# Kernel tuning notes

Measured on AMD Instinct MI355X. Metric: run time of the kernel, lower is better.

Reference implementation:

```python
import jax, jax.numpy as jnp
import numpy as np

D = 256; H = 8; FF = 1024; Q = 128; C = 512; B = 4
HD = D // H

def _ln(x, g, b):
    m = x.mean(-1, keepdims=True)
    v = ((x - m) ** 2).mean(-1, keepdims=True)
    return (x - m) / jnp.sqrt(v + 1e-5) * g + b

def _mha(q, k, v, in_w, in_b, out_w, out_b):
    # q,k,v: (L,B,D) / (S,B,D); in_w: (3D,D) packed q|k|v as in torch MHA
    qp = q @ in_w[:D].T + in_b[:D]
    kp = k @ in_w[D:2*D].T + in_b[D:2*D]
    vp = v @ in_w[2*D:].T + in_b[2*D:]
    L, Bb, _ = qp.shape; S = kp.shape[0]
    qh = qp.reshape(L, Bb, H, HD)
    kh = kp.reshape(S, Bb, H, HD)
    vh = vp.reshape(S, Bb, H, HD)
    scores = jnp.einsum('lbhd,sbhd->bhls', qh, kh) / np.sqrt(HD).astype(np.float32)
    a = jax.nn.softmax(scores, axis=-1)
    o = jnp.einsum('bhls,sbhd->lbhd', a, vh).reshape(L, Bb, D)
    return o @ out_w.T + out_b

def setup_inputs() -> dict:
    key = jax.random.key(0)
    ks = jax.random.split(key, 30)
    def p(k, shape, s=0.02):
        return jax.random.normal(k, shape, jnp.float32) * s
    return {
        'tgt': jax.random.normal(ks[0], (Q, B, D), jnp.float32),
        'memory': jax.random.normal(ks[1], (C, B, D), jnp.float32),
        'query_pos': jax.random.normal(ks[2], (Q, B, D), jnp.float32),
        'relative_pos': jax.random.normal(ks[3], (Q, C, B, D), jnp.float32),
        'ln1_g': jnp.ones((D,), jnp.float32), 'ln1_b': jnp.zeros((D,), jnp.float32),
        'ln2_g': jnp.ones((D,), jnp.float32), 'ln2_b': jnp.zeros((D,), jnp.float32),
        'ln3_g': jnp.ones((D,), jnp.float32), 'ln3_b': jnp.zeros((D,), jnp.float32),
        'in_proj_w': p(ks[4], (3 * D, D)), 'in_proj_b': jnp.zeros((3 * D,), jnp.float32),
        'attn_out_w': p(ks[5], (D, D)), 'attn_out_b': jnp.zeros((D,), jnp.float32),
        'mlp1_w': p(ks[6], (D, D)), 'mlp1_b': jnp.zeros((D,), jnp.float32),
        'mlp2_w': p(ks[7], (D, D)), 'mlp2_b': jnp.zeros((D,), jnp.float32),
        'v_w': p(ks[8], (D, D)), 'v_b': jnp.zeros((D,), jnp.float32),
        'o_w': p(ks[9], (D, D)), 'o_b': jnp.zeros((D,), jnp.float32),
        'ff1_w': p(ks[10], (FF, D)), 'ff1_b': jnp.zeros((FF,), jnp.float32),
        'ff2_w': p(ks[11], (D, FF)), 'ff2_b': jnp.zeros((D,), jnp.float32),
    }

def reference(tgt, memory, query_pos, relative_pos,
              ln1_g, ln1_b, ln2_g, ln2_b, ln3_g, ln3_b,
              in_proj_w, in_proj_b, attn_out_w, attn_out_b,
              mlp1_w, mlp1_b, mlp2_w, mlp2_b,
              v_w, v_b, o_w, o_b, ff1_w, ff1_b, ff2_w, ff2_b):
    # pre-norm self-attention (dropout = identity in eval)
    tgt2 = _ln(tgt, ln1_g, ln1_b)
    qk = tgt2 + query_pos
    sa = _mha(qk, qk, tgt2, in_proj_w, in_proj_b, attn_out_w, attn_out_b)
    tgt = tgt + sa
    # relation-attention branch
    tgt2 = _ln(tgt, ln2_g, ln2_b)                       # (Q,B,D)
    x = tgt2[:, None, :, :] - memory[None, :, :, :] + relative_pos  # (Q,C,B,D)
    h = jax.nn.relu(x @ mlp1_w.T + mlp1_b)
    sim = h @ mlp2_w.T + mlp2_b                          # (Q,C,B,D)
    attn = jax.nn.softmax(sim / np.sqrt(D).astype(np.float32), axis=1)
    v2 = (memory[None, :, :, :] + relative_pos) @ v_w.T + v_b
    t = jnp.einsum('qcbf,qcbf->qbf', attn, v2)           # (Q,B,D)
    t = jax.nn.relu(t @ o_w.T + o_b)
    tgt = t + tgt2
    # FFN
    tgt2 = _ln(tgt, ln3_g, ln3_b)
    ff = jax.nn.relu(tgt2 @ ff1_w.T + ff1_b) @ ff2_w.T + ff2_b
    return tgt + ff
```

## Files before the change

### kernel.cpp

```cpp
#include <hip/hip_runtime.h>
#include <hip/hip_bf16.h>
#include <cstdint>
#include <cstddef>

#define DEV __device__ __forceinline__

typedef __attribute__((ext_vector_type(8))) short short8;
typedef __attribute__((ext_vector_type(4))) float f32x4;

constexpr int Dm  = 256;
constexpr int Qn  = 128;
constexpr int Cn  = 512;
constexpr int Bn  = 4;

DEV unsigned short f2bf(float f){
  unsigned int u = __builtin_bit_cast(unsigned int, f);
  u += 0x7fffu + ((u >> 16) & 1u);
  return (unsigned short)(u >> 16);
}
DEV float bfl(unsigned int u){ return __builtin_bit_cast(float, u << 16); }
DEV float bfh(unsigned int u){ return __builtin_bit_cast(float, u & 0xffff0000u); }
DEV unsigned int pk2(float a, float b){
  return (unsigned int)f2bf(a) | ((unsigned int)f2bf(b) << 16);
}
DEV unsigned int corr2(unsigned int x, unsigned int m, unsigned int t){
  return pk2(bfl(x) + bfl(m) - bfl(t), bfh(x) + bfh(m) - bfh(t));
}

DEV f32x4 mfma16(short8 a, short8 b, f32x4 c){
  return __builtin_amdgcn_mfma_f32_16x16x32_bf16(a, b, c, 0, 0, 0);
}

DEV short8 ldfrag(const unsigned short* buf, int rowbytes, int row0, int ks, int l){
  int r = row0 + (l & 15);
  int byte = (ks * 64 + ((l >> 4) * 16)) ^ ((r & 7) << 4);
  return *(const short8*)((const char*)buf + r * rowbytes + byte);
}

DEV void gload_lds16(const void* g, void* lds){
  __builtin_amdgcn_global_load_lds(
      (const __attribute__((address_space(1))) unsigned int*)g,
      (__attribute__((address_space(3))) unsigned int*)lds, 16, 0, 0);
}

DEV void packw(unsigned short* dst, const float* src, int j){
  int f = j >> 8, d = j & 255;
  int d8 = d >> 3, e = d & 7;
  int byte = (d8 * 16) ^ ((f & 15) << 4);
  dst[f * 256 + (byte >> 1) + e] = f2bf(src[j]);
}

__global__ __launch_bounds__(256) void conv_all_kernel(
    const float* inw, unsigned short* inw_bf,
    const float* aow, unsigned short* aow_bf,
    const float* ow,  unsigned short* ow_bf,
    const float* f1w, unsigned short* f1w_bf,
    const float* f2w, unsigned short* f2w_bf,
    const float* m1w, unsigned short* w1pk,
    const float* m2w, unsigned short* w2pk,
    const float* vw,  unsigned short* wvpk,
    const float* memp, unsigned short* m2r)
{
  const int total = 196608 + 65536 + 65536 + 262144 + 262144 + 3 * 65536 + 524288;
  for (int i = blockIdx.x * 256 + threadIdx.x; i < total; i += gridDim.x * 256){
    int j = i;
    if (j < 196608){ inw_bf[j] = f2bf(inw[j]); continue; } j -= 196608;
    if (j < 65536) { aow_bf[j] = f2bf(aow[j]); continue; } j -= 65536;
    if (j < 65536) { ow_bf[j]  = f2bf(ow[j]);  continue; } j -= 65536;
    if (j < 262144){ f1w_bf[j] = f2bf(f1w[j]); continue; } j -= 262144;
    if (j < 262144){ f2w_bf[j] = f2bf(f2w[j]); continue; } j -= 262144;
    if (j < 65536) { packw(w1pk, m1w, j); continue; } j -= 65536;
    if (j < 65536) { packw(w2pk, m2w, j); continue; } j -= 65536;
    if (j < 65536) { packw(wvpk, vw, j);  continue; } j -= 65536;
    int d = j & 255, c = (j >> 8) & 511, b2 = j >> 17;
    m2r[j] = f2bf(2.f * memp[((size_t)c * 4 + b2) * 256 + d]);
  }
}

__global__ __launch_bounds__(256) void xprep_kernel(
    const float* __restrict__ rel, const float* __restrict__ memp,
    const float* __restrict__ t22, unsigned short* __restrict__ xg)
{
  const int total = Qn * Cn * Bn * 32;
  for (int i = blockIdx.x * 256 + threadIdx.x; i < total; i += gridDim.x * 256){
    int d8 = i & 31;
    int b  = (i >> 5) & 3;
    int c  = (i >> 7) & 511;
    int q  = i >> 16;
    const float4* rp = (const float4*)(rel + (size_t)i * 8);
    float4 r0 = rp[0], r1 = rp[1];
    const float4* mp = (const float4*)(memp + ((size_t)(c * 4 + b) * 256 + d8 * 8));
    float4 m0 = mp[0], m1 = mp[1];
    const float4* tp = (const float4*)(t22 + ((size_t)(q * 4 + b) * 256 + d8 * 8));
    float4 t0 = tp[0], t1 = tp[1];
    uint4 o;
    o.x = pk2(t0.x - m0.x + r0.x, t0.y - m0.y + r0.y);
    o.y = pk2(t0.z - m0.z + r0.z, t0.w - m0.w + r0.w);
    o.z = pk2(t1.x - m1.x + r1.x, t1.y - m1.y + r1.y);
    o.w = pk2(t1.z - m1.z + r1.z, t1.w - m1.w + r1.w);
    size_t byte = ((size_t)(q * 4 + b) * 512 + c) * 512 + ((d8 * 16) ^ ((c & 15) << 4));
    *(uint4*)((char*)xg + byte) = o;
  }
}

__global__ __launch_bounds__(256) void ln_kernel(
    const float* __restrict__ in, const float* __restrict__ g, const float* __restrict__ bt,
    const float* __restrict__ addp,
    float* __restrict__ outF, unsigned short* __restrict__ outA, unsigned short* __restrict__ outB)
{
  const int r = blockIdx.x, t = threadIdx.x;
  float x = in[(size_t)r * 256 + t];
  float s = x, s2 = x * x;
  #pragma unroll
  for (int m = 1; m < 64; m <<= 1){ s += __shfl_xor(s, m, 64); s2 += __shfl_xor(s2, m, 64); }
  __shared__ float ls[8];
  int w = t >> 6, l = t & 63;
  if (l == 0){ ls[w] = s; ls[4 + w] = s2; }
  __syncthreads();
  s  = ls[0] + ls[1] + ls[2] + ls[3];
  s2 = ls[4] + ls[5] + ls[6] + ls[7];
  float mean = s * (1.f / 256.f);
  float var  = s2 * (1.f / 256.f) - mean * mean;
  float y = (x - mean) * rsqrtf(var + 1e-5f) * g[t] + bt[t];
  size_t o = (size_t)r * 256 + t;
  if (outF) outF[o] = y;
  if (outA) outA[o] = f2bf(y);
  if (outB) outB[o] = f2bf(y + addp[o]);
}

__global__ __launch_bounds__(256, 4) void gemm_kernel(
    const unsigned short* __restrict__ A, const unsigned short* __restrict__ W,
    const float* __restrict__ bias, const float* __restrict__ resid,
    float* __restrict__ Cf, unsigned short* __restrict__ Cb,
    int M, int N, int K, float alpha, int relu)
{
  __shared__ unsigned short As[64 * 64];
  __shared__ unsigned short Ws[64 * 64];
  const int tid = threadIdx.x;
  const int l = tid & 63;
  const int w = tid >> 6;
  const int wm = w >> 1, wn = w & 1;
  const int bm = blockIdx.x * 64, bn = blockIdx.y * 64;
  f32x4 acc[2][2] = {{{0,0,0,0},{0,0,0,0}},{{0,0,0,0},{0,0,0,0}}};

  for (int kc = 0; kc < K; kc += 64){
    __syncthreads();
    #pragma unroll
    for (int i = 0; i < 2; ++i){
      int idx = tid + i * 256;
      int r = idx >> 3, s = idx & 7;
      int byte = (s * 16) ^ ((r & 7) << 4);
      *(short8*)((char*)As + r * 128 + byte) = *(const short8*)(A + (size_t)(bm + r) * K + kc + s * 8);
      *(short8*)((char*)Ws + r * 128 + byte) = *(const short8*)(W + (size_t)(bn + r) * K + kc + s * 8);
    }
    __syncthreads();
    #pragma unroll
    for (int ks = 0; ks < 2; ++ks){
      short8 af[2], bf[2];
      af[0] = ldfrag(As, 128, wm * 32,      ks, l);
      af[1] = ldfrag(As, 128, wm * 32 + 16, ks, l);
      bf[0] = ldfrag(Ws, 128, wn * 32,      ks, l);
      bf[1] = ldfrag(Ws, 128, wn * 32 + 16, ks, l);
      #pragma unroll
      for (int i = 0; i < 2; ++i)
        #pragma unroll
        for (int j = 0; j < 2; ++j)
          acc[i][j] = mfma16(af[i], bf[j], acc[i][j]);
    }
  }
  #pragma unroll
  for (int i = 0; i < 2; ++i)
  #pragma unroll
  for (int j = 0; j < 2; ++j){
    int col = bn + wn * 32 + j * 16 + (l & 15);
    float bv = bias ? bias[col] : 0.f;
    #pragma unroll
    for (int u = 0; u < 4; ++u){
      int row = bm + wm * 32 + i * 16 + ((l >> 4) << 2) + u;
      float v = alpha * acc[i][j][u] + bv;
      if (relu) v = fmaxf(v, 0.f);
      if (resid) v += resid[(size_t)row * N + col];
      if (Cf) Cf[(size_t)row * N + col] = v;
      if (Cb) Cb[(size_t)row * N + col] = f2bf(v);
    }
  }
}

__global__ __launch_bounds__(256) void attn_kernel(
    const float* __restrict__ qkp, const float* __restrict__ vp,
    unsigned short* __restrict__ attn_o)
{
  __shared__ float ks[128][33];
  __shared__ float vs[128][33];
  __shared__ float sc[128][129];
  const int bh = blockIdx.x;
  const int b = bh >> 3, h = bh & 7;
  const int tid = threadIdx.x;
  const int lrow = tid >> 1;
  const int half = tid & 1;
  {
    int s = tid >> 1;
    int d0 = half * 16;
    const float* kp = qkp + ((size_t)s * Bn + b) * 512 + 256 + h * 32 + d0;
    const float* vv = vp  + ((size_t)s * Bn + b) * 256 +       h * 32 + d0;
    #pragma unroll
    for (int d = 0; d < 16; d += 4){
      *(float4*)&ks[s][d0 + d] = *(const float4*)(kp + d);
      *(float4*)&vs[s][d0 + d] = *(const float4*)(vv + d);
    }
  }
  __syncthreads();
  float qv[32];
  const float* qp = qkp + ((size_t)lrow * Bn + b) * 512 + h * 32;
  #pragma unroll
  for (int d = 0; d < 32; ++d) qv[d] = qp[d];
  const float scale = 0.17677669529663687f;
  float mloc = -1e30f;
  for (int s2 = 0; s2 < 64; ++s2){
    int s = half * 64 + s2;
    float dot = 0.f;
    #pragma unroll
    for (int d = 0; d < 32; ++d) dot += qv[d] * ks[s][d];
    dot *= scale;
    sc[lrow][s] = dot;
    mloc = fmaxf(mloc, dot);
  }
  float m = fmaxf(mloc, __shfl_xor(mloc, 1, 64));
  float sum = 0.f;
  for (int s2 = 0; s2 < 64; ++s2){
    int s = half * 64 + s2;
    float e = __expf(sc[lrow][s] - m);
    sum += e;
    sc[lrow][s] = e;
  }
  sum += __shfl_xor(sum, 1, 64);
  float inv = 1.f / sum;
  float o[32];
  #pragma unroll
  for (int d = 0; d < 32; ++d) o[d] = 0.f;
  for (int s2 = 0; s2 < 64; ++s2){
    int s = half * 64 + s2;
    float e = sc[lrow][s];
    #pragma unroll
    for (int d = 0; d < 32; ++d) o[d] += e * vs[s][d];
  }
  #pragma unroll
  for (int d = 0; d < 32; ++d){
    o[d] += __shfl_xor(o[d], 1, 64);
    o[d] *= inv;
  }
  unsigned short* op = attn_o + ((size_t)lrow * Bn + b) * 256 + h * 32 + half * 16;
  #pragma unroll
  for (int d = 0; d < 16; ++d) op[d] = f2bf(o[half * 16 + d]);
}

template<int MODE>
__global__ __launch_bounds__(1024, 4) void relpass_kernel(
    const unsigned short* src, const unsigned short* __restrict__ Wg,
    const float* __restrict__ bias, unsigned short* dst,
    const unsigned short* __restrict__ m2r, const unsigned short* __restrict__ t22b,
    const unsigned short* simsrc)
{
  __shared__ unsigned short Wt[65536];
  __shared__ unsigned short xb[8192];
  const int qb = blockIdx.x;
  const int b = qb & 3;
  const int tid = threadIdx.x;
  const int w = tid >> 6, l = tid & 63;
  const int ch2 = w >> 3, fb = w & 7;
  const int l15 = l & 15, lg = l >> 4;

  #pragma unroll
  for (int i = 0; i < 8; ++i){
    int base = w * 64 + i * 1024;
    gload_lds16((const char*)Wg + ((size_t)base + l) * 16, (char*)Wt + (size_t)base * 16);
  }

  const int row = tid >> 5, d8 = tid & 31;
  const int toff = row * 512 + ((d8 * 16) ^ ((row & 15) << 4));
  const char* srcp = (const char*)src + (size_t)qb * 262144;

  uint4 stg = *(const uint4*)(srcp + toff);
  uint4 m2c, t2c;
  if constexpr (MODE == 2){
    m2c = *(const uint4*)((const char*)m2r + ((size_t)(b * 512 + row) * 512) + d8 * 16);
    t2c = *(const uint4*)((const char*)t22b + (size_t)qb * 512 + d8 * 16);
  }
  asm volatile("s_waitcnt vmcnt(0)" ::: "memory");
  if constexpr (MODE == 2){
    stg.x = corr2(stg.x, m2c.x, t2c.x);
    stg.y = corr2(stg.y, m2c.y, t2c.y);
    stg.z = corr2(stg.z, m2c.z, t2c.z);
    stg.w = corr2(stg.w, m2c.w, t2c.w);
  }
  *(uint4*)((char*)xb + toff) = stg;
  __syncthreads();

  float bv[2][4];
  #pragma unroll
  for (int j = 0; j < 2; ++j)
    #pragma unroll
    for (int u = 0; u < 4; ++u)
      bv[j][u] = bias[fb * 32 + j * 16 + lg * 4 + u];

  float ta[2][4], la[2][4];
  if constexpr (MODE == 2){
    #pragma unroll
    for (int j = 0; j < 2; ++j)
      #pragma unroll
      for (int u = 0; u < 4; ++u){ ta[j][u] = 0.f; la[j][u] = 0.f; }
  }

  const int r = ch2 * 16 + l15;
  for (int t = 0; t < 16; ++t){
    if (t < 15){
      stg = *(const uint4*)(srcp + (size_t)(t + 1) * 16384 + toff);
      if constexpr (MODE == 2)
        m2c = *(const uint4*)((const char*)m2r + ((size_t)(b * 512 + (t + 1) * 32 + row) * 512) + d8 * 16);
    }
    uint4 simv;
    if constexpr (MODE == 2)
      simv = *(const uint4*)((const char*)simsrc + (size_t)qb * 262144 + (size_t)t * 16384 + (size_t)(w * 64 + l) * 16);

    f32x4 acc[2] = {{0,0,0,0},{0,0,0,0}};
    #pragma unroll
    for (int kc = 0; kc < 8; ++kc){
      short8 bx = *(const short8*)((const char*)xb + r * 512 + ((kc * 64 + lg * 16) ^ ((r & 15) << 4)));
      #pragma unroll
      for (int j = 0; j < 2; ++j){
        int f = fb * 32 + j * 16 + l15;
        short8 aw = *(const short8*)((const char*)Wt + f * 512 + ((kc * 64 + lg * 16) ^ ((f & 15) << 4)));
        acc[j] = mfma16(aw, bx, acc[j]);
      }
    }

    if constexpr (MODE == 0){
      int c = t * 32 + r;
      size_t rowb = (size_t)qb * 262144 + (size_t)c * 512;
      #pragma unroll
      for (int j = 0; j < 2; ++j){
        uint2 pk;
        pk.x = pk2(fmaxf(acc[j][0] + bv[j][0], 0.f), fmaxf(acc[j][1] + bv[j][1], 0.f));
        pk.y = pk2(fmaxf(acc[j][2] + bv[j][2], 0.f), fmaxf(acc[j][3] + bv[j][3], 0.f));
        int inrow = (fb * 64 + j * 32 + lg * 8) ^ ((c & 15) << 4);
        *(uint2*)((char*)dst + rowb + inrow) = pk;
      }
    } else if constexpr (MODE == 1){
      uint4 d;
      d.x = pk2((acc[0][0] + bv[0][0]) * 0.0625f, (acc[0][1] + bv[0][1]) * 0.0625f);
      d.y = pk2((acc[0][2] + bv[0][2]) * 0.0625f, (acc[0][3] + bv[0][3]) * 0.0625f);
      d.z = pk2((acc[1][0] + bv[1][0]) * 0.0625f, (acc[1][1] + bv[1][1]) * 0.0625f);
      d.w = pk2((acc[1][2] + bv[1][2]) * 0.0625f, (acc[1][3] + bv[1][3]) * 0.0625f);
      *(uint4*)((char*)dst + (size_t)qb * 262144 + (size_t)t * 16384 + (size_t)(w * 64 + l) * 16) = d;
    } else {
      const unsigned int sv[4] = {simv.x, simv.y, simv.z, simv.w};
      #pragma unroll
      for (int j = 0; j < 2; ++j)
        #pragma unroll
        for (int p = 0; p < 2; ++p){
          unsigned int s2 = sv[j * 2 + p];
          float e0 = __expf(bfl(s2)), e1 = __expf(bfh(s2));
          float v0 = acc[j][p * 2 + 0] + bv[j][p * 2 + 0];
          float v1 = acc[j][p * 2 + 1] + bv[j][p * 2 + 1];
          ta[j][p * 2 + 0] += e0 * v0;  la[j][p * 2 + 0] += e0;
          ta[j][p * 2 + 1] += e1 * v1;  la[j][p * 2 + 1] += e1;
        }
    }

    if (t < 15){
      __syncthreads();
      if constexpr (MODE == 2){
        stg.x = corr2(stg.x, m2c.x, t2c.x);
        stg.y = corr2(stg.y, m2c.y, t2c.y);
        stg.z = corr2(stg.z, m2c.z, t2c.z);
        stg.w = corr2(stg.w, m2c.w, t2c.w);
      }
      *(uint4*)((char*)xb + toff) = stg;
      __syncthreads();
    }
  }

  if constexpr (MODE == 2){
    #pragma unroll
    for (int j = 0; j < 2; ++j)
      #pragma unroll
      for (int u = 0; u < 4; ++u){
        #pragma unroll
        for (int m = 1; m <= 8; m <<= 1){
          ta[j][u] += __shfl_xor(ta[j][u], m, 64);
          la[j][u] += __shfl_xor(la[j][u], m, 64);
        }
      }
    __syncthreads();
    float* bufT = (float*)xb;
    float* bufL = bufT + 512;
    if (l15 == 0){
      #pragma unroll
      for (int j = 0; j < 2; ++j)
        #pragma unroll
        for (int u = 0; u < 4; ++u){
          int f = fb * 32 + j * 16 + lg * 4 + u;
          bufT[ch2 * 256 + f] = ta[j][u];
          bufL[ch2 * 256 + f] = la[j][u];
        }
    }
    __syncthreads();
    if (tid < 256){
      float T = bufT[tid] + bufT[256 + tid];
      float L = bufL[tid] + bufL[256 + tid];
      dst[(size_t)qb * 256 + tid] = f2bf(T / L);
    }
  }
}

extern "C" void kernel_launch(void* const* d_in, const int* in_sizes, int n_in,
                              void* d_out, int out_size, void* d_ws, size_t ws_size,
                              hipStream_t stream)
{
  const float* tgt  = (const float*)d_in[0];
  const float* mem  = (const float*)d_in[1];
  const float* qpos = (const float*)d_in[2];
  const float* rel  = (const float*)d_in[3];
  const float* ln1g = (const float*)d_in[4];
  const float* ln1b = (const float*)d_in[5];
  const float* ln2g = (const float*)d_in[6];
  const float* ln2b = (const float*)d_in[7];
  const float* ln3g = (const float*)d_in[8];
  const float* ln3b = (const float*)d_in[9];
  const float* inw  = (const float*)d_in[10];
  const float* inb  = (const float*)d_in[11];
  const float* aow  = (const float*)d_in[12];
  const float* aob  = (const float*)d_in[13];
  const float* m1w  = (const float*)d_in[14];
  const float* m1b  = (const float*)d_in[15];
  const float* m2w  = (const float*)d_in[16];
  const float* m2b  = (const float*)d_in[17];
  const float* vw   = (const float*)d_in[18];
  const float* vb   = (const float*)d_in[19];
  const float* ow   = (const float*)d_in[20];
  const float* ob   = (const float*)d_in[21];
  const float* f1w  = (const float*)d_in[22];
  const float* f1b  = (const float*)d_in[23];
  const float* f2w  = (const float*)d_in[24];
  const float* f2b  = (const float*)d_in[25];

  char* ws = (char*)d_ws;
  size_t off = 0;
  auto alloc = [&](size_t bytes) -> char* {
    char* p = ws + off; off += (bytes + 255) & ~size_t(255); return p;
  };
  unsigned short* x_sw    = (unsigned short*)alloc((size_t)512 * 512 * 256 * 2);
  unsigned short* h_sw    = (unsigned short*)alloc((size_t)512 * 512 * 256 * 2);
  unsigned short* m2r     = (unsigned short*)alloc(4 * 512 * 256 * 2);
  unsigned short* w1pk    = (unsigned short*)alloc(256 * 256 * 2);
  unsigned short* w2pk    = (unsigned short*)alloc(256 * 256 * 2);
  unsigned short* wvpk    = (unsigned short*)alloc(256 * 256 * 2);
  unsigned short* inw_bf  = (unsigned short*)alloc(768 * 256 * 2);
  unsigned short* aow_bf  = (unsigned short*)alloc(256 * 256 * 2);
  unsigned short* ow_bf   = (unsigned short*)alloc(256 * 256 * 2);
  unsigned short* f1w_bf  = (unsigned short*)alloc(1024 * 256 * 2);
  unsigned short* f2w_bf  = (unsigned short*)alloc(256 * 1024 * 2);
  unsigned short* t21_bf  = (unsigned short*)alloc(512 * 256 * 2);
  unsigned short* qk_bf   = (unsigned short*)alloc(512 * 256 * 2);
  float*          qkp     = (float*)alloc(512 * 512 * 4);
  float*          vp      = (float*)alloc(512 * 256 * 4);
  unsigned short* ao_bf   = (unsigned short*)alloc(512 * 256 * 2);
  float*          tgta    = (float*)alloc(512 * 256 * 4);
  float*          t22_f   = (float*)alloc(512 * 256 * 4);
  unsigned short* t22_bf  = (unsigned short*)alloc(512 * 256 * 2);
  unsigned short* trel_bf = (unsigned short*)alloc(512 * 256 * 2);
  float*          tgtr    = (float*)alloc(512 * 256 * 4);
  unsigned short* t23_bf  = (unsigned short*)alloc(512 * 256 * 2);
  unsigned short* ffh_bf  = (unsigned short*)alloc(512 * 1024 * 2);

  conv_all_kernel<<<2048, 256, 0, stream>>>(inw, inw_bf, aow, aow_bf, ow, ow_bf,
      f1w, f1w_bf, f2w, f2w_bf, m1w, w1pk, m2w, w2pk, vw, wvpk, mem, m2r);

  ln_kernel<<<512, 256, 0, stream>>>(tgt, ln1g, ln1b, qpos, nullptr, t21_bf, qk_bf);

  gemm_kernel<<<dim3(8, 8), 256, 0, stream>>>(qk_bf, inw_bf, inb, nullptr,
      qkp, nullptr, 512, 512, 256, 1.f, 0);
  gemm_kernel<<<dim3(8, 4), 256, 0, stream>>>(t21_bf, inw_bf + 512 * 256, inb + 512, nullptr,
      vp, nullptr, 512, 256, 256, 1.f, 0);

  attn_kernel<<<32, 256, 0, stream>>>(qkp, vp, ao_bf);

  gemm_kernel<<<dim3(8, 4), 256, 0, stream>>>(ao_bf, aow_bf, aob, tgt,
      tgta, nullptr, 512, 256, 256, 1.f, 0);

  ln_kernel<<<512, 256, 0, stream>>>(tgta, ln2g, ln2b, nullptr, t22_f, t22_bf, nullptr);

  xprep_kernel<<<2048, 256, 0, stream>>>(rel, mem, t22_f, x_sw);

  relpass_kernel<0><<<512, 1024, 0, stream>>>(x_sw, w1pk, m1b, h_sw, nullptr, nullptr, nullptr);
  relpass_kernel<1><<<512, 1024, 0, stream>>>(h_sw, w2pk, m2b, h_sw, nullptr, nullptr, nullptr);
  relpass_kernel<2><<<512, 1024, 0, stream>>>(x_sw, wvpk, vb, trel_bf, m2r, t22_bf, h_sw);

  gemm_kernel<<<dim3(8, 4), 256, 0, stream>>>(trel_bf, ow_bf, ob, t22_f,
      tgtr, nullptr, 512, 256, 256, 1.f, 1);

  ln_kernel<<<512, 256, 0, stream>>>(tgtr, ln3g, ln3b, nullptr, nullptr, t23_bf, nullptr);

  gemm_kernel<<<dim3(8, 16), 256, 0, stream>>>(t23_bf, f1w_bf, f1b, nullptr,
      nullptr, ffh_bf, 512, 1024, 256, 1.f, 1);
  gemm_kernel<<<dim3(8, 4), 256, 0, stream>>>(ffh_bf, f2w_bf, f2b, tgtr,
      (float*)d_out, nullptr, 512, 256, 1024, 1.f, 0);
}
```

Before: 401.6 us.

## Fuse x/y input prep into first relation pass, drop xprep kernel

New measurement: 373.3 us. 1.08x faster.

```diff
diff --git a/kernel.cpp b/kernel.cpp
--- a/kernel.cpp
+++ b/kernel.cpp
@@ -22,9 +22,6 @@
 DEV float bfh(unsigned int u){ return __builtin_bit_cast(float, u & 0xffff0000u); }
 DEV unsigned int pk2(float a, float b){
   return (unsigned int)f2bf(a) | ((unsigned int)f2bf(b) << 16);
-}
-DEV unsigned int corr2(unsigned int x, unsigned int m, unsigned int t){
-  return pk2(bfl(x) + bfl(m) - bfl(t), bfh(x) + bfh(m) - bfh(t));
 }
 
 DEV f32x4 mfma16(short8 a, short8 b, f32x4 c){
@@ -58,10 +55,9 @@
     const float* f2w, unsigned short* f2w_bf,
     const float* m1w, unsigned short* w1pk,
     const float* m2w, unsigned short* w2pk,
-    const float* vw,  unsigned short* wvpk,
-    const float* memp, unsigned short* m2r)
+    const float* vw,  unsigned short* wvpk)
 {
-  const int total = 196608 + 65536 + 65536 + 262144 + 262144 + 3 * 65536 + 524288;
+  const int total = 196608 + 65536 + 65536 + 262144 + 262144 + 3 * 65536;
   for (int i = blockIdx.x * 256 + threadIdx.x; i < total; i += gridDim.x * 256){
     int j = i;
     if (j < 196608){ inw_bf[j] = f2bf(inw[j]); continue; } j -= 196608;
@@ -71,35 +67,7 @@
     if (j < 262144){ f2w_bf[j] = f2bf(f2w[j]); continue; } j -= 262144;
     if (j < 65536) { packw(w1pk, m1w, j); continue; } j -= 65536;
     if (j < 65536) { packw(w2pk, m2w, j); continue; } j -= 65536;
-    if (j < 65536) { packw(wvpk, vw, j);  continue; } j -= 65536;
-    int d = j & 255, c = (j >> 8) & 511, b2 = j >> 17;
-    m2r[j] = f2bf(2.f * memp[((size_t)c * 4 + b2) * 256 + d]);
-  }
-}
-
-__global__ __launch_bounds__(256) void xprep_kernel(
-    const float* __restrict__ rel, const float* __restrict__ memp,
-    const float* __restrict__ t22, unsigned short* __restrict__ xg)
-{
-  const int total = Qn * Cn * Bn * 32;
-  for (int i = blockIdx.x * 256 + threadIdx.x; i < total; i += gridDim.x * 256){
-    int d8 = i & 31;
-    int b  = (i >> 5) & 3;
-    int c  = (i >> 7) & 511;
-    int q  = i >> 16;
-    const float4* rp = (const float4*)(rel + (size_t)i * 8);
-    float4 r0 = rp[0], r1 = rp[1];
-    const float4* mp = (const float4*)(memp + ((size_t)(c * 4 + b) * 256 + d8 * 8));
-    float4 m0 = mp[0], m1 = mp[1];
-    const float4* tp = (const float4*)(t22 + ((size_t)(q * 4 + b) * 256 + d8 * 8));
-    float4 t0 = tp[0], t1 = tp[1];
-    uint4 o;
-    o.x = pk2(t0.x - m0.x + r0.x, t0.y - m0.y + r0.y);
-    o.y = pk2(t0.z - m0.z + r0.z, t0.w - m0.w + r0.w);
-    o.z = pk2(t1.x - m1.x + r1.x, t1.y - m1.y + r1.y);
-    o.w = pk2(t1.z - m1.z + r1.z, t1.w - m1.w + r1.w);
-    size_t byte = ((size_t)(q * 4 + b) * 512 + c) * 512 + ((d8 * 16) ^ ((c & 15) << 4));
-    *(uint4*)((char*)xg + byte) = o;
+    packw(wvpk, vw, j);
   }
 }
 
@@ -256,15 +224,16 @@
 
 template<int MODE>
 __global__ __launch_bounds__(1024, 4) void relpass_kernel(
+    const float* __restrict__ rel, const float* __restrict__ memp,
+    const float* __restrict__ t22f,
     const unsigned short* src, const unsigned short* __restrict__ Wg,
     const float* __restrict__ bias, unsigned short* dst,
-    const unsigned short* __restrict__ m2r, const unsigned short* __restrict__ t22b,
-    const unsigned short* simsrc)
+    unsigned short* ydst, const unsigned short* __restrict__ simsrc)
 {
   __shared__ unsigned short Wt[65536];
   __shared__ unsigned short xb[8192];
   const int qb = blockIdx.x;
-  const int b = qb & 3;
+  const int q = qb >> 2, b = qb & 3;
   const int tid = threadIdx.x;
   const int w = tid >> 6, l = tid & 63;
   const int ch2 = w >> 3, fb = w & 7;
@@ -280,20 +249,35 @@
   const int toff = row * 512 + ((d8 * 16) ^ ((row & 15) << 4));
   const char* srcp = (const char*)src + (size_t)qb * 262144;
 
-  uint4 stg = *(const uint4*)(srcp + toff);
-  uint4 m2c, t2c;
-  if constexpr (MODE == 2){
-    m2c = *(const uint4*)((const char*)m2r + ((size_t)(b * 512 + row) * 512) + d8 * 16);
-    t2c = *(const uint4*)((const char*)t22b + (size_t)qb * 512 + d8 * 16);
+  float4 t20, t21;
+  float4 r0, r1, m0, m1;
+  uint4 stg;
+  if constexpr (MODE == 0){
+    t20 = *(const float4*)(t22f + (size_t)qb * 256 + d8 * 8);
+    t21 = *(const float4*)(t22f + (size_t)qb * 256 + d8 * 8 + 4);
+    const float* rp = rel + (((size_t)q * 512 + row) * 4 + b) * 256 + d8 * 8;
+    const float* mp = memp + ((size_t)(row * 4 + b)) * 256 + d8 * 8;
+    r0 = *(const float4*)rp;  r1 = *(const float4*)(rp + 4);
+    m0 = *(const float4*)mp;  m1 = *(const float4*)(mp + 4);
+  } else {
+    stg = *(const uint4*)(srcp + toff);
   }
   asm volatile("s_waitcnt vmcnt(0)" ::: "memory");
-  if constexpr (MODE == 2){
-    stg.x = corr2(stg.x, m2c.x, t2c.x);
-    stg.y = corr2(stg.y, m2c.y, t2c.y);
-    stg.z = corr2(stg.z, m2c.z, t2c.z);
-    stg.w = corr2(stg.w, m2c.w, t2c.w);
-  }
-  *(uint4*)((char*)xb + toff) = stg;
+  if constexpr (MODE == 0){
+    uint4 xw, yw;
+    xw.x = pk2(t20.x - m0.x + r0.x, t20.y - m0.y + r0.y);
+    xw.y = pk2(t20.z - m0.z + r0.z, t20.w - m0.w + r0.w);
+    xw.z = pk2(t21.x - m1.x + r1.x, t21.y - m1.y + r1.y);
+    xw.w = pk2(t21.z - m1.z + r1.z, t21.w - m1.w + r1.w);
+    yw.x = pk2(r0.x + m0.x, r0.y + m0.y);
+    yw.y = pk2(r0.z + m0.z, r0.w + m0.w);
+    yw.z = pk2(r1.x + m1.x, r1.y + m1.y);
+    yw.w = pk2(r1.z + m1.z, r1.w + m1.w);
+    *(uint4*)((char*)ydst + (size_t)qb * 262144 + toff) = yw;
+    *(uint4*)((char*)xb + toff) = xw;
+  } else {
+    *(uint4*)((char*)xb + toff) = stg;
+  }
   __syncthreads();
 
   float bv[2][4];
@@ -314,9 +298,15 @@
   const int r = ch2 * 16 + l15;
   for (int t = 0; t < 16; ++t){
     if (t < 15){
-      stg = *(const uint4*)(srcp + (size_t)(t + 1) * 16384 + toff);
-      if constexpr (MODE == 2)
-        m2c = *(const uint4*)((const char*)m2r + ((size_t)(b * 512 + (t + 1) * 32 + row) * 512) + d8 * 16);
+      if constexpr (MODE == 0){
+        int c = (t + 1) * 32 + row;
+        const float* rp = rel + (((size_t)q * 512 + c) * 4 + b) * 256 + d8 * 8;
+        const float* mp = memp + ((size_t)(c * 4 + b)) * 256 + d8 * 8;
+        r0 = *(const float4*)rp;  r1 = *(const float4*)(rp + 4);
+        m0 = *(const float4*)mp;  m1 = *(const float4*)(mp + 4);
+      } else {
+        stg = *(const uint4*)(srcp + (size_t)(t + 1) * 16384 + toff);
+      }
     }
     uint4 simv;
     if constexpr (MODE == 2)
@@ -369,13 +359,21 @@
 
     if (t < 15){
       __syncthreads();
-      if constexpr (MODE == 2){
-        stg.x = corr2(stg.x, m2c.x, t2c.x);
-        stg.y = corr2(stg.y, m2c.y, t2c.y);
-        stg.z = corr2(stg.z, m2c.z, t2c.z);
-        stg.w = corr2(stg.w, m2c.w, t2c.w);
+      if constexpr (MODE == 0){
+        uint4 xw, yw;
+        xw.x = pk2(t20.x - m0.x + r0.x, t20.y - m0.y + r0.y);
+        xw.y = pk2(t20.z - m0.z + r0.z, t20.w - m0.w + r0.w);
+        xw.z = pk2(t21.x - m1.x + r1.x, t21.y - m1.y + r1.y);
+        xw.w = pk2(t21.z - m1.z + r1.z, t21.w - m1.w + r1.w);
+        yw.x = pk2(r0.x + m0.x, r0.y + m0.y);
+        yw.y = pk2(r0.z + m0.z, r0.w + m0.w);
+        yw.z = pk2(r1.x + m1.x, r1.y + m1.y);
+        yw.w = pk2(r1.z + m1.z, r1.w + m1.w);
+        *(uint4*)((char*)ydst + (size_t)qb * 262144 + (size_t)(t + 1) * 16384 + toff) = yw;
+        *(uint4*)((char*)xb + toff) = xw;
+      } else {
+        *(uint4*)((char*)xb + toff) = stg;
       }
-      *(uint4*)((char*)xb + toff) = stg;
       __syncthreads();
     }
   }
@@ -449,9 +447,8 @@
   auto alloc = [&](size_t bytes) -> char* {
     char* p = ws + off; off += (bytes + 255) & ~size_t(255); return p;
   };
-  unsigned short* x_sw    = (unsigned short*)alloc((size_t)512 * 512 * 256 * 2);
+  unsigned short* y_sw    = (unsigned short*)alloc((size_t)512 * 512 * 256 * 2);
   unsigned short* h_sw    = (unsigned short*)alloc((size_t)512 * 512 * 256 * 2);
-  unsigned short* m2r     = (unsigned short*)alloc(4 * 512 * 256 * 2);
   unsigned short* w1pk    = (unsigned short*)alloc(256 * 256 * 2);
   unsigned short* w2pk    = (unsigned short*)alloc(256 * 256 * 2);
   unsigned short* wvpk    = (unsigned short*)alloc(256 * 256 * 2);
@@ -467,14 +464,13 @@
   unsigned short* ao_bf   = (unsigned short*)alloc(512 * 256 * 2);
   float*          tgta    = (float*)alloc(512 * 256 * 4);
   float*          t22_f   = (float*)alloc(512 * 256 * 4);
-  unsigned short* t22_bf  = (unsigned short*)alloc(512 * 256 * 2);
   unsigned short* trel_bf = (unsigned short*)alloc(512 * 256 * 2);
   float*          tgtr    = (float*)alloc(512 * 256 * 4);
   unsigned short* t23_bf  = (unsigned short*)alloc(512 * 256 * 2);
   unsigned short* ffh_bf  = (unsigned short*)alloc(512 * 1024 * 2);
 
   conv_all_kernel<<<2048, 256, 0, stream>>>(inw, inw_bf, aow, aow_bf, ow, ow_bf,
-      f1w, f1w_bf, f2w, f2w_bf, m1w, w1pk, m2w, w2pk, vw, wvpk, mem, m2r);
+      f1w, f1w_bf, f2w, f2w_bf, m1w, w1pk, m2w, w2pk, vw, wvpk);
 
   ln_kernel<<<512, 256, 0, stream>>>(tgt, ln1g, ln1b, qpos, nullptr, t21_bf, qk_bf);
 
@@ -488,13 +484,14 @@
   gemm_kernel<<<dim3(8, 4), 256, 0, stream>>>(ao_bf, aow_bf, aob, tgt,
       tgta, nullptr, 512, 256, 256, 1.f, 0);
 
-  ln_kernel<<<512, 256, 0, stream>>>(tgta, ln2g, ln2b, nullptr, t22_f, t22_bf, nullptr);
-
-  xprep_kernel<<<2048, 256, 0, stream>>>(rel, mem, t22_f, x_sw);
-
-  relpass_kernel<0><<<512, 1024, 0, stream>>>(x_sw, w1pk, m1b, h_sw, nullptr, nullptr, nullptr);
-  relpass_kernel<1><<<512, 1024, 0, stream>>>(h_sw, w2pk, m2b, h_sw, nullptr, nullptr, nullptr);
-  relpass_kernel<2><<<512, 1024, 0, stream>>>(x_sw, wvpk, vb, trel_bf, m2r, t22_bf, h_sw);
+  ln_kernel<<<512, 256, 0, stream>>>(tgta, ln2g, ln2b, nullptr, t22_f, nullptr, nullptr);
+
+  relpass_kernel<0><<<512, 1024, 0, stream>>>(rel, mem, t22_f, nullptr, w1pk, m1b,
+      h_sw, y_sw, nullptr);
+  relpass_kernel<1><<<512, 1024, 0, stream>>>(nullptr, nullptr, nullptr, h_sw, w2pk, m2b,
+      h_sw, nullptr, nullptr);
+  relpass_kernel<2><<<512, 1024, 0, stream>>>(nullptr, nullptr, nullptr, y_sw, wvpk, vb,
+      trel_bf, nullptr, h_sw);
 
   gemm_kernel<<<dim3(8, 4), 256, 0, stream>>>(trel_bf, ow_bf, ob, t22_f,
       tgtr, nullptr, 512, 256, 256, 1.f, 1);
```
